# Kernel tuning notes

Measured on AMD Instinct MI355X. Metric: run time of the kernel, lower is better.

The kernel has to match this reference:

```python
import jax, jax.numpy as jnp
import numpy as np

H = 16       # num heads
HD = 64      # head dim
D = H * HD   # hidden size

def _rotate_half(x):
    x1, x2 = jnp.split(x, 2, axis=-1)
    return jnp.concatenate([-x2, x1], axis=-1)

def setup_inputs() -> dict:
    key = jax.random.key(0)
    ks = jax.random.split(key, 12)
    B, N, NP = 16, 1029, 1024  # batch, tokens (5 prefix + 1024 patches), patch tokens
    inp = {
        "hidden_states": jax.random.normal(ks[0], (B, N, D), dtype=jnp.float32),
        "sin": jax.random.uniform(ks[1], (NP, HD), dtype=jnp.float32, minval=-1.0, maxval=1.0),
        "cos": jax.random.uniform(ks[2], (NP, HD), dtype=jnp.float32, minval=-1.0, maxval=1.0),
        "Wq": jax.random.normal(ks[3], (D, D), dtype=jnp.float32) * 0.02,
        "bq": jnp.zeros((D,), dtype=jnp.float32),
        "Wk": jax.random.normal(ks[4], (D, D), dtype=jnp.float32) * 0.02,
        "bk": jnp.zeros((D,), dtype=jnp.float32),
        "Wv": jax.random.normal(ks[5], (D, D), dtype=jnp.float32) * 0.02,
        "bv": jnp.zeros((D,), dtype=jnp.float32),
        "Wo": jax.random.normal(ks[6], (D, D), dtype=jnp.float32) * 0.02,
        "bo": jnp.zeros((D,), dtype=jnp.float32),
    }
    return inp

def reference(hidden_states, sin, cos, Wq, bq, Wk, bk, Wv, bv, Wo, bo):
    B, N, _ = hidden_states.shape
    scaling = HD ** -0.5
    # qkv projections (nn.Linear: x @ W.T + b), split to heads: [B,H,N,HD]
    def proj(W, b):
        y = hidden_states @ W.T + b
        return y.reshape(B, N, H, HD).transpose(0, 2, 1, 3)
    q, k, v = proj(Wq, bq), proj(Wk, bk), proj(Wv, bv)
    # rotary pos emb on patch-token suffix only
    prefix = N - sin.shape[-2]
    def rope(x):
        xs = x[:, :, prefix:, :]
        xs = xs * cos + _rotate_half(xs) * sin
        return jnp.concatenate([x[:, :, :prefix, :], xs], axis=2)
    q, k = rope(q), rope(k)
    # eager attention: softmax in fp32
    attn = jnp.einsum("bhqd,bhkd->bhqk", q, k) * scaling
    attn = jax.nn.softmax(attn.astype(jnp.float32), axis=-1).astype(q.dtype)
    out = jnp.einsum("bhqk,bhkd->bhqd", attn, v)
    out = out.transpose(0, 2, 1, 3).reshape(B, N, D)
    return out @ Wo.T + bo
```

## Files before the change

### kernel.cpp

```cpp
#include <hip/hip_runtime.h>
#include <stdint.h>

#define H 16
#define HD 64
#define D 1024
#define NTOK 1029
#define BATCH 16
#define NPAD 1152
#define M_ROWS (BATCH*NTOK)
#define MPAD 16512
#define KB 1024
#define PREFIX 5

typedef unsigned short u16;
typedef __attribute__((ext_vector_type(8))) short short8;
typedef __attribute__((ext_vector_type(4))) short short4v;
typedef __attribute__((ext_vector_type(4))) float float4v;
typedef __attribute__((ext_vector_type(4))) unsigned int uint4v;

__device__ __forceinline__ u16 f2bf(float x) {
  unsigned int u = __float_as_uint(x);
  u += 0x7FFFu + ((u >> 16) & 1u);
  return (u16)(u >> 16);
}

__device__ __forceinline__ void gload16(const void* g, void* l) {
  __builtin_amdgcn_global_load_lds((const __attribute__((address_space(1))) void*)g,
                                   (__attribute__((address_space(3))) void*)l, 16, 0, 0);
}

__global__ __launch_bounds__(256) void cvt_A_kernel(const float* __restrict__ src,
                                                    u16* __restrict__ dst) {
  int idx = blockIdx.x * 256 + threadIdx.x;
  int m = idx >> 8, k = (idx & 255) * 4;
  float4v x = (float4v)0.f;
  if (m < M_ROWS) x = *(const float4v*)(src + (size_t)m * D + k);
  short4v o;
#pragma unroll
  for (int j = 0; j < 4; j++) o[j] = (short)f2bf(x[j]);
  *(short4v*)(dst + (size_t)m * D + k) = o;
}

__global__ __launch_bounds__(256) void cvt_W_kernel(
    const float* __restrict__ w0, const float* __restrict__ w1,
    const float* __restrict__ w2, const float* __restrict__ w3,
    u16* __restrict__ e0, u16* __restrict__ e1, u16* __restrict__ e2, u16* __restrict__ e3) {
  const float* src = (blockIdx.y == 0) ? w0 : (blockIdx.y == 1) ? w1 : (blockIdx.y == 2) ? w2 : w3;
  u16* dst = (blockIdx.y == 0) ? e0 : (blockIdx.y == 1) ? e1 : (blockIdx.y == 2) ? e2 : e3;
  int idx = blockIdx.x * 256 + threadIdx.x;
  int m = idx >> 8, k = (idx & 255) * 4;
  float4v x = *(const float4v*)(src + (size_t)m * D + k);
  short4v o;
#pragma unroll
  for (int j = 0; j < 4; j++) o[j] = (short)f2bf(x[j]);
  *(short4v*)(dst + (size_t)m * D + k) = o;
}

__device__ __forceinline__ void gemm_mainloop(const u16* __restrict__ A,
                                              const u16* __restrict__ Bw,
                                              u16* As, u16* Bs,
                                              int mtile, int ntile,
                                              float4v acc[4][4]) {
  const int tid = threadIdx.x;
  const int lane = tid & 63;
  const int wave = tid >> 6;
  const int wm = (wave >> 1) * 64;
  const int wn = (wave & 1) * 64;
  const int ar = lane & 15;
  const int kq = lane >> 4;
#pragma unroll
  for (int i = 0; i < 4; i++)
#pragma unroll
    for (int j = 0; j < 4; j++) acc[i][j] = (float4v)0.f;

  const size_t abase = (size_t)mtile * 128 * KB;
  const size_t bbase = (size_t)ntile * 128 * KB;
  for (int k0 = 0; k0 < KB; k0 += 64) {
    __syncthreads();
#pragma unroll
    for (int h = 0; h < 2; h++) {
#pragma unroll
      for (int i = 0; i < 2; i++) {
        int chunk = i * 256 + tid;
        gload16(A + abase + (size_t)(chunk >> 2) * KB + k0 + h * 32 + (chunk & 3) * 8,
                As + h * 4096 + (size_t)(i * 256 + (tid & ~63)) * 8);
        gload16(Bw + bbase + (size_t)(chunk >> 2) * KB + k0 + h * 32 + (chunk & 3) * 8,
                Bs + h * 4096 + (size_t)(i * 256 + (tid & ~63)) * 8);
      }
    }
    __syncthreads();
#pragma unroll
    for (int h = 0; h < 2; h++) {
      short8 af[4], bf[4];
#pragma unroll
      for (int ms = 0; ms < 4; ms++)
        af[ms] = *(const short8*)(As + h * 4096 + (wm + ms * 16 + ar) * 32 + kq * 8);
#pragma unroll
      for (int ns = 0; ns < 4; ns++)
        bf[ns] = *(const short8*)(Bs + h * 4096 + (wn + ns * 16 + ar) * 32 + kq * 8);
#pragma unroll
      for (int ms = 0; ms < 4; ms++)
#pragma unroll
        for (int ns = 0; ns < 4; ns++)
          acc[ms][ns] = __builtin_amdgcn_mfma_f32_16x16x32_bf16(af[ms], bf[ns], acc[ms][ns], 0, 0, 0);
    }
  }
}

__global__ __launch_bounds__(256) void gemm_qkv_kernel(
    const u16* __restrict__ A,
    const u16* __restrict__ Wqb, const u16* __restrict__ Wkb, const u16* __restrict__ Wvb,
    const float* __restrict__ bq, const float* __restrict__ bk, const float* __restrict__ bv,
    const float* __restrict__ sinp, const float* __restrict__ cosp,
    u16* __restrict__ qb, u16* __restrict__ kb, u16* __restrict__ vt) {
  __shared__ __align__(16) u16 As[2 * 128 * 32];
  __shared__ __align__(16) u16 Bs[2 * 128 * 32];
  int L = blockIdx.x;
  int t = (L & 7) * 387 + (L >> 3);
  int z = t / 1032;
  int r = t - z * 1032;
  const int mtile = r >> 3, ntile = r & 7;
  const u16* Bw = (z == 0) ? Wqb : (z == 1) ? Wkb : Wvb;
  const float* bias = (z == 0) ? bq : (z == 1) ? bk : bv;
  float4v acc[4][4];
  gemm_mainloop(A, Bw, As, Bs, mtile, ntile, acc);

  const int tid = threadIdx.x, lane = tid & 63, wave = tid >> 6;
  const int wm = (wave >> 1) * 64, wn = (wave & 1) * 64;
  const int ar = lane & 15, kq = lane >> 4;
#pragma unroll
  for (int ms = 0; ms < 4; ms++) {
#pragma unroll
    for (int r2 = 0; r2 < 4; r2++) {
      int grow = mtile * 128 + wm + ms * 16 + kq * 4 + r2;
      if (grow >= M_ROWS) continue;
      int b = grow / NTOK;
      int n = grow - b * NTOK;
      bool dorope = (z != 2) && (n >= PREFIX);
      int pos = n - PREFIX;
#pragma unroll
      for (int ns = 0; ns < 4; ns++) {
        int col = ntile * 128 + wn + ns * 16 + ar;
        int hh = col >> 6, d = col & 63;
        float y = acc[ms][ns][r2] + bias[col];
        if (z == 2) {
          vt[((size_t)(b * H + hh) * 64 + d) * NPAD + n] = f2bf(y);
          continue;
        }
        if (dorope) {
          float xp = acc[ms][ns ^ 2][r2] + bias[col ^ 32];
          float c = cosp[pos * HD + d], s = sinp[pos * HD + d];
          y = y * c + ((d < 32) ? -xp : xp) * s;
        }
        if (z == 0) y *= 0.125f;
        u16* outp = (z == 0) ? qb : kb;
        outp[((size_t)(b * H + hh) * NPAD + n) * 64 + d] = f2bf(y);
      }
    }
  }
}

#define SSHIFT 3.0f
#define NJT 17
__global__ __launch_bounds__(256) void attn_kernel(const u16* __restrict__ qb,
                                                   const u16* __restrict__ kb,
                                                   const u16* __restrict__ vt,
                                                   u16* __restrict__ ao) {
  __shared__ __align__(16) u16 sQ[128 * 72];
  __shared__ __align__(16) u16 sK[64 * 72];
  __shared__ __align__(16) u16 sV[64 * 72];
  const int tid = threadIdx.x, lane = tid & 63, wave = tid >> 6;
  const int ar = lane & 15, kq = lane >> 4;
  const int qt = blockIdx.x, hh = blockIdx.y, b = blockIdx.z;
  const int bh = b * H + hh;
  const u16* qbase = qb + (size_t)bh * NPAD * 64;
  const u16* kbase = kb + (size_t)bh * NPAD * 64;
  const u16* vbase = vt + (size_t)bh * 64 * NPAD;

#pragma unroll
  for (int i = 0; i < 4; i++) {
    int chunk = i * 256 + tid;
    int row = chunk >> 3, c = chunk & 7;
    *(uint4v*)(sQ + row * 72 + c * 8) =
        *(const uint4v*)(qbase + (size_t)(qt * 128 + row) * 64 + c * 8);
  }
  __syncthreads();
  short8 aq[2][2];
#pragma unroll
  for (int ms = 0; ms < 2; ms++)
#pragma unroll
    for (int ki = 0; ki < 2; ki++)
      aq[ms][ki] = *(const short8*)(sQ + (wave * 32 + ms * 16 + ar) * 72 + ki * 32 + kq * 8);
  u16* sP = sQ + wave * 32 * 72;

  float rs[2][4];
  float4v o_acc[2][4];
#pragma unroll
  for (int ms = 0; ms < 2; ms++)
#pragma unroll
    for (int r = 0; r < 4; r++) rs[ms][r] = 0.f;
#pragma unroll
  for (int ms = 0; ms < 2; ms++)
#pragma unroll
    for (int t = 0; t < 4; t++) o_acc[ms][t] = (float4v)0.f;

  for (int jt = 0; jt < NJT; jt++) {
    __syncthreads();
#pragma unroll
    for (int i = 0; i < 2; i++) {
      int chunk = i * 256 + tid;
      int row = chunk >> 3, c = chunk & 7;
      *(uint4v*)(sK + row * 72 + c * 8) =
          *(const uint4v*)(kbase + (size_t)(jt * 64 + row) * 64 + c * 8);
      *(uint4v*)(sV + row * 72 + c * 8) =
          *(const uint4v*)(vbase + (size_t)row * NPAD + jt * 64 + c * 8);
    }
    __syncthreads();

    float4v s[2][4];
#pragma unroll
    for (int ms = 0; ms < 2; ms++)
#pragma unroll
      for (int t = 0; t < 4; t++) s[ms][t] = (float4v)0.f;
#pragma unroll
    for (int ki = 0; ki < 2; ki++) {
#pragma unroll
      for (int t = 0; t < 4; t++) {
        short8 bk8 = *(const short8*)(sK + (t * 16 + ar) * 72 + ki * 32 + kq * 8);
#pragma unroll
        for (int ms = 0; ms < 2; ms++)
          s[ms][t] = __builtin_amdgcn_mfma_f32_16x16x32_bf16(aq[ms][ki], bk8, s[ms][t], 0, 0, 0);
      }
    }
    if (jt == NJT - 1) {
#pragma unroll
      for (int t = 0; t < 4; t++)
        if ((NJT - 1) * 64 + t * 16 + ar >= NTOK) {
#pragma unroll
          for (int ms = 0; ms < 2; ms++) s[ms][t] = (float4v)(-INFINITY);
        }
    }
    asm volatile("" ::: "memory");
#pragma unroll
    for (int ms = 0; ms < 2; ms++)
#pragma unroll
      for (int t = 0; t < 4; t++)
#pragma unroll
        for (int r = 0; r < 4; r++) {
          float p = __expf(s[ms][t][r] - SSHIFT);
          rs[ms][r] += p;
          sP[(ms * 16 + kq * 4 + r) * 72 + t * 16 + ar] = f2bf(p);
        }
    asm volatile("" ::: "memory");
#pragma unroll
    for (int ki = 0; ki < 2; ki++) {
#pragma unroll
      for (int ms = 0; ms < 2; ms++) {
        short8 ap = *(const short8*)(sP + (ms * 16 + ar) * 72 + ki * 32 + kq * 8);
#pragma unroll
        for (int t = 0; t < 4; t++) {
          short8 bv8 = *(const short8*)(sV + (t * 16 + ar) * 72 + ki * 32 + kq * 8);
          o_acc[ms][t] = __builtin_amdgcn_mfma_f32_16x16x32_bf16(ap, bv8, o_acc[ms][t], 0, 0, 0);
        }
      }
    }
  }
#pragma unroll
  for (int ms = 0; ms < 2; ms++)
#pragma unroll
    for (int r = 0; r < 4; r++) {
      float l = rs[ms][r];
#pragma unroll
      for (int off = 1; off < 16; off <<= 1) l += __shfl_xor(l, off, 64);
      int i = qt * 128 + wave * 32 + ms * 16 + kq * 4 + r;
      if (i >= NTOK) continue;
      float inv = 1.f / l;
      size_t mg = (size_t)b * NTOK + i;
#pragma unroll
      for (int t = 0; t < 4; t++)
        ao[mg * D + hh * 64 + t * 16 + ar] = f2bf(o_acc[ms][t][r] * inv);
    }
}

__global__ __launch_bounds__(256) void gemm_o_kernel(const u16* __restrict__ A,
                                                     const u16* __restrict__ Wob,
                                                     const float* __restrict__ bo,
                                                     float* __restrict__ out) {
  __shared__ __align__(16) u16 As[2 * 128 * 32];
  __shared__ __align__(16) u16 Bs[2 * 128 * 32];
  int L = blockIdx.x;
  int t = (L & 7) * 129 + (L >> 3);
  const int mtile = t >> 3, ntile = t & 7;
  float4v acc[4][4];
  gemm_mainloop(A, Wob, As, Bs, mtile, ntile, acc);
  const int tid = threadIdx.x, lane = tid & 63, wave = tid >> 6;
  const int wm = (wave >> 1) * 64, wn = (wave & 1) * 64;
  const int ar = lane & 15, kq = lane >> 4;
#pragma unroll
  for (int ms = 0; ms < 4; ms++)
#pragma unroll
    for (int r = 0; r < 4; r++) {
      int grow = mtile * 128 + wm + ms * 16 + kq * 4 + r;
      if (grow >= M_ROWS) continue;
#pragma unroll
      for (int ns = 0; ns < 4; ns++) {
        int col = ntile * 128 + wn + ns * 16 + ar;
        out[(size_t)grow * D + col] = acc[ms][ns][r] + bo[col];
      }
    }
}

extern "C" void kernel_launch(void* const* d_in, const int* in_sizes, int n_in,
                              void* d_out, int out_size, void* d_ws, size_t ws_size,
                              hipStream_t stream) {
  const float* hidden = (const float*)d_in[0];
  const float* sinp = (const float*)d_in[1];
  const float* cosp = (const float*)d_in[2];
  const float* Wq = (const float*)d_in[3]; const float* bq = (const float*)d_in[4];
  const float* Wk = (const float*)d_in[5]; const float* bk = (const float*)d_in[6];
  const float* Wv = (const float*)d_in[7]; const float* bv = (const float*)d_in[8];
  const float* Wo = (const float*)d_in[9]; const float* bo = (const float*)d_in[10];
  float* out = (float*)d_out;
  (void)in_sizes; (void)n_in; (void)out_size; (void)ws_size;

  char* ws = (char*)d_ws;
  size_t off = 0;
  auto carve = [&](size_t elems) {
    u16* p = (u16*)(ws + off);
    off += ((elems * 2 + 255) & ~(size_t)255);
    return p;
  };
  u16* A_bf = carve((size_t)MPAD * KB);
  u16* Wqb = carve((size_t)D * KB);
  u16* Wkb = carve((size_t)D * KB);
  u16* Wvb = carve((size_t)D * KB);
  u16* Wob = carve((size_t)D * KB);
  u16* q_b = carve((size_t)BATCH * H * NPAD * 64);
  u16* k_b = carve((size_t)BATCH * H * NPAD * 64);
  u16* v_t = carve((size_t)BATCH * H * NPAD * 64);

  hipLaunchKernelGGL(cvt_A_kernel, dim3(MPAD), dim3(256), 0, stream, hidden, A_bf);
  hipLaunchKernelGGL(cvt_W_kernel, dim3(1024, 4), dim3(256), 0, stream,
                     Wq, Wk, Wv, Wo, Wqb, Wkb, Wvb, Wob);
  hipLaunchKernelGGL(gemm_qkv_kernel, dim3(3096), dim3(256), 0, stream,
                     A_bf, Wqb, Wkb, Wvb, bq, bk, bv, sinp, cosp, q_b, k_b, v_t);
  hipLaunchKernelGGL(attn_kernel, dim3(9, H, BATCH), dim3(256), 0, stream, q_b, k_b, v_t, A_bf);
  hipLaunchKernelGGL(gemm_o_kernel, dim3(1032), dim3(256), 0, stream, A_bf, Wob, bo, out);
}
```

Measured before the change: 621.1 us.

## Store operands in MFMA fragment layout and load GEMM fragments directly from global

The conversion kernels and the attention output now write A and the weights in a pre-swizzled 16-row by 32-k fragment order, and the Q/K/V weights are packed into one buffer. The GEMM mainloop drops shared memory and barriers and loads each wave's MFMA fragments straight from global memory with register double buffering. The goal is to remove LDS staging and sync overhead. The cost is that operand reuse across waves in a block no longer happens on-chip, so L2 traffic per block increases. Block-to-tile mapping for the QKV GEMM is also changed to group N tiles per XCD.

```diff
diff --git a/kernel.cpp b/kernel.cpp
--- a/kernel.cpp
+++ b/kernel.cpp
@@ -24,10 +24,6 @@
   return (u16)(u >> 16);
 }
 
-__device__ __forceinline__ void gload16(const void* g, void* l) {
-  __builtin_amdgcn_global_load_lds((const __attribute__((address_space(1))) void*)g,
-                                   (__attribute__((address_space(3))) void*)l, 16, 0, 0);
-}
 
 __global__ __launch_bounds__(256) void cvt_A_kernel(const float* __restrict__ src,
                                                     u16* __restrict__ dst) {
@@ -38,96 +34,96 @@
   short4v o;
 #pragma unroll
   for (int j = 0; j < 4; j++) o[j] = (short)f2bf(x[j]);
-  *(short4v*)(dst + (size_t)m * D + k) = o;
+  int gm = m >> 4, rm = m & 15, gk = k >> 5, kq = (k >> 3) & 3, e = k & 7;
+  size_t off = (((size_t)gm * 32 + gk) * 64 + (rm + 16 * kq)) * 8 + e;
+  *(short4v*)(dst + off) = o;
 }
 
 __global__ __launch_bounds__(256) void cvt_W_kernel(
     const float* __restrict__ w0, const float* __restrict__ w1,
     const float* __restrict__ w2, const float* __restrict__ w3,
-    u16* __restrict__ e0, u16* __restrict__ e1, u16* __restrict__ e2, u16* __restrict__ e3) {
-  const float* src = (blockIdx.y == 0) ? w0 : (blockIdx.y == 1) ? w1 : (blockIdx.y == 2) ? w2 : w3;
-  u16* dst = (blockIdx.y == 0) ? e0 : (blockIdx.y == 1) ? e1 : (blockIdx.y == 2) ? e2 : e3;
+    u16* __restrict__ wqkv, u16* __restrict__ wo) {
+  const int y = blockIdx.y;
+  const float* src = (y == 0) ? w0 : (y == 1) ? w1 : (y == 2) ? w2 : w3;
   int idx = blockIdx.x * 256 + threadIdx.x;
   int m = idx >> 8, k = (idx & 255) * 4;
   float4v x = *(const float4v*)(src + (size_t)m * D + k);
   short4v o;
 #pragma unroll
   for (int j = 0; j < 4; j++) o[j] = (short)f2bf(x[j]);
-  *(short4v*)(dst + (size_t)m * D + k) = o;
-}
-
-__device__ __forceinline__ void gemm_mainloop(const u16* __restrict__ A,
-                                              const u16* __restrict__ Bw,
-                                              u16* As, u16* Bs,
-                                              int mtile, int ntile,
-                                              float4v acc[4][4]) {
-  const int tid = threadIdx.x;
-  const int lane = tid & 63;
-  const int wave = tid >> 6;
-  const int wm = (wave >> 1) * 64;
-  const int wn = (wave & 1) * 64;
-  const int ar = lane & 15;
-  const int kq = lane >> 4;
+  int gn = (y == 3) ? (m >> 4) : (y * 64 + (m >> 4));
+  int rn = m & 15, gk = k >> 5, kq = (k >> 3) & 3, e = k & 7;
+  u16* dst = (y == 3) ? wo : wqkv;
+  size_t off = (((size_t)gn * 32 + gk) * 64 + (rn + 16 * kq)) * 8 + e;
+  *(short4v*)(dst + off) = o;
+}
+
+__device__ __forceinline__ void gemm_frag_mainloop(const u16* __restrict__ A2,
+                                                   const u16* __restrict__ B2,
+                                                   int gm0, int gn0, int lane,
+                                                   float4v acc[4][4]) {
+  const u16* pa[4];
+  const u16* pb[4];
+#pragma unroll
+  for (int i = 0; i < 4; i++) {
+    pa[i] = A2 + (size_t)(gm0 + i) * (32 * 512) + lane * 8;
+    pb[i] = B2 + (size_t)(gn0 + i) * (32 * 512) + lane * 8;
+  }
 #pragma unroll
   for (int i = 0; i < 4; i++)
 #pragma unroll
     for (int j = 0; j < 4; j++) acc[i][j] = (float4v)0.f;
 
-  const size_t abase = (size_t)mtile * 128 * KB;
-  const size_t bbase = (size_t)ntile * 128 * KB;
-  for (int k0 = 0; k0 < KB; k0 += 64) {
-    __syncthreads();
-#pragma unroll
-    for (int h = 0; h < 2; h++) {
-#pragma unroll
-      for (int i = 0; i < 2; i++) {
-        int chunk = i * 256 + tid;
-        gload16(A + abase + (size_t)(chunk >> 2) * KB + k0 + h * 32 + (chunk & 3) * 8,
-                As + h * 4096 + (size_t)(i * 256 + (tid & ~63)) * 8);
-        gload16(Bw + bbase + (size_t)(chunk >> 2) * KB + k0 + h * 32 + (chunk & 3) * 8,
-                Bs + h * 4096 + (size_t)(i * 256 + (tid & ~63)) * 8);
-      }
-    }
-    __syncthreads();
-#pragma unroll
-    for (int h = 0; h < 2; h++) {
-      short8 af[4], bf[4];
-#pragma unroll
-      for (int ms = 0; ms < 4; ms++)
-        af[ms] = *(const short8*)(As + h * 4096 + (wm + ms * 16 + ar) * 32 + kq * 8);
+  short8 a0[4], b0[4], a1[4], b1[4];
+#pragma unroll
+  for (int i = 0; i < 4; i++) {
+    a0[i] = *(const short8*)(pa[i]);
+    b0[i] = *(const short8*)(pb[i]);
+  }
+#pragma unroll 2
+  for (int gk = 0; gk < 32; gk += 2) {
+#pragma unroll
+    for (int i = 0; i < 4; i++) {
+      a1[i] = *(const short8*)(pa[i] + (gk + 1) * 512);
+      b1[i] = *(const short8*)(pb[i] + (gk + 1) * 512);
+    }
+#pragma unroll
+    for (int ms = 0; ms < 4; ms++)
 #pragma unroll
       for (int ns = 0; ns < 4; ns++)
-        bf[ns] = *(const short8*)(Bs + h * 4096 + (wn + ns * 16 + ar) * 32 + kq * 8);
-#pragma unroll
-      for (int ms = 0; ms < 4; ms++)
-#pragma unroll
-        for (int ns = 0; ns < 4; ns++)
-          acc[ms][ns] = __builtin_amdgcn_mfma_f32_16x16x32_bf16(af[ms], bf[ns], acc[ms][ns], 0, 0, 0);
-    }
+        acc[ms][ns] = __builtin_amdgcn_mfma_f32_16x16x32_bf16(a0[ms], b0[ns], acc[ms][ns], 0, 0, 0);
+    if (gk + 2 < 32) {
+#pragma unroll
+      for (int i = 0; i < 4; i++) {
+        a0[i] = *(const short8*)(pa[i] + (gk + 2) * 512);
+        b0[i] = *(const short8*)(pb[i] + (gk + 2) * 512);
+      }
+    }
+#pragma unroll
+    for (int ms = 0; ms < 4; ms++)
+#pragma unroll
+      for (int ns = 0; ns < 4; ns++)
+        acc[ms][ns] = __builtin_amdgcn_mfma_f32_16x16x32_bf16(a1[ms], b1[ns], acc[ms][ns], 0, 0, 0);
   }
 }
 
 __global__ __launch_bounds__(256) void gemm_qkv_kernel(
-    const u16* __restrict__ A,
-    const u16* __restrict__ Wqb, const u16* __restrict__ Wkb, const u16* __restrict__ Wvb,
+    const u16* __restrict__ A2, const u16* __restrict__ Wqkv,
     const float* __restrict__ bq, const float* __restrict__ bk, const float* __restrict__ bv,
     const float* __restrict__ sinp, const float* __restrict__ cosp,
     u16* __restrict__ qb, u16* __restrict__ kb, u16* __restrict__ vt) {
-  __shared__ __align__(16) u16 As[2 * 128 * 32];
-  __shared__ __align__(16) u16 Bs[2 * 128 * 32];
-  int L = blockIdx.x;
-  int t = (L & 7) * 387 + (L >> 3);
-  int z = t / 1032;
-  int r = t - z * 1032;
-  const int mtile = r >> 3, ntile = r & 7;
-  const u16* Bw = (z == 0) ? Wqb : (z == 1) ? Wkb : Wvb;
+  const int L = blockIdx.x;
+  const int xcd = L & 7, i = L >> 3;
+  const int lt = i % 3, mtile = i / 3;
+  const int ntile = xcd * 3 + lt;
+  const int z = ntile >> 3;
   const float* bias = (z == 0) ? bq : (z == 1) ? bk : bv;
-  float4v acc[4][4];
-  gemm_mainloop(A, Bw, As, Bs, mtile, ntile, acc);
-
   const int tid = threadIdx.x, lane = tid & 63, wave = tid >> 6;
   const int wm = (wave >> 1) * 64, wn = (wave & 1) * 64;
   const int ar = lane & 15, kq = lane >> 4;
+  float4v acc[4][4];
+  gemm_frag_mainloop(A2, Wqkv, mtile * 8 + (wm >> 4), ntile * 8 + (wn >> 4), lane, acc);
+
 #pragma unroll
   for (int ms = 0; ms < 4; ms++) {
 #pragma unroll
@@ -140,7 +136,7 @@
       int pos = n - PREFIX;
 #pragma unroll
       for (int ns = 0; ns < 4; ns++) {
-        int col = ntile * 128 + wn + ns * 16 + ar;
+        int col = (ntile & 7) * 128 + wn + ns * 16 + ar;
         int hh = col >> 6, d = col & 63;
         float y = acc[ms][ns][r2] + bias[col];
         if (z == 2) {
@@ -275,27 +271,28 @@
       int i = qt * 128 + wave * 32 + ms * 16 + kq * 4 + r;
       if (i >= NTOK) continue;
       float inv = 1.f / l;
-      size_t mg = (size_t)b * NTOK + i;
-#pragma unroll
-      for (int t = 0; t < 4; t++)
-        ao[mg * D + hh * 64 + t * 16 + ar] = f2bf(o_acc[ms][t][r] * inv);
-    }
-}
-
-__global__ __launch_bounds__(256) void gemm_o_kernel(const u16* __restrict__ A,
-                                                     const u16* __restrict__ Wob,
+      int m = b * NTOK + i;
+      int gm = m >> 4, rm = m & 15;
+#pragma unroll
+      for (int t = 0; t < 4; t++) {
+        int col = hh * 64 + t * 16 + ar;
+        int gk = col >> 5, kqp = (col >> 3) & 3, e = col & 7;
+        ao[(((size_t)gm * 32 + gk) * 64 + (rm + 16 * kqp)) * 8 + e] = f2bf(o_acc[ms][t][r] * inv);
+      }
+    }
+}
+
+__global__ __launch_bounds__(256) void gemm_o_kernel(const u16* __restrict__ A2,
+                                                     const u16* __restrict__ Wo2,
                                                      const float* __restrict__ bo,
                                                      float* __restrict__ out) {
-  __shared__ __align__(16) u16 As[2 * 128 * 32];
-  __shared__ __align__(16) u16 Bs[2 * 128 * 32];
-  int L = blockIdx.x;
-  int t = (L & 7) * 129 + (L >> 3);
-  const int mtile = t >> 3, ntile = t & 7;
-  float4v acc[4][4];
-  gemm_mainloop(A, Wob, As, Bs, mtile, ntile, acc);
+  const int L = blockIdx.x;
+  const int ntile = L & 7, mtile = L >> 3;
   const int tid = threadIdx.x, lane = tid & 63, wave = tid >> 6;
   const int wm = (wave >> 1) * 64, wn = (wave & 1) * 64;
   const int ar = lane & 15, kq = lane >> 4;
+  float4v acc[4][4];
+  gemm_frag_mainloop(A2, Wo2, mtile * 8 + (wm >> 4), ntile * 8 + (wn >> 4), lane, acc);
 #pragma unroll
   for (int ms = 0; ms < 4; ms++)
 #pragma unroll
@@ -330,20 +327,18 @@
     off += ((elems * 2 + 255) & ~(size_t)255);
     return p;
   };
-  u16* A_bf = carve((size_t)MPAD * KB);
-  u16* Wqb = carve((size_t)D * KB);
-  u16* Wkb = carve((size_t)D * KB);
-  u16* Wvb = carve((size_t)D * KB);
-  u16* Wob = carve((size_t)D * KB);
+  u16* A_fg = carve((size_t)MPAD * KB);
+  u16* Wqkv = carve((size_t)3 * D * KB);
+  u16* Wo2 = carve((size_t)D * KB);
   u16* q_b = carve((size_t)BATCH * H * NPAD * 64);
   u16* k_b = carve((size_t)BATCH * H * NPAD * 64);
   u16* v_t = carve((size_t)BATCH * H * NPAD * 64);
 
-  hipLaunchKernelGGL(cvt_A_kernel, dim3(MPAD), dim3(256), 0, stream, hidden, A_bf);
+  hipLaunchKernelGGL(cvt_A_kernel, dim3(MPAD), dim3(256), 0, stream, hidden, A_fg);
   hipLaunchKernelGGL(cvt_W_kernel, dim3(1024, 4), dim3(256), 0, stream,
-                     Wq, Wk, Wv, Wo, Wqb, Wkb, Wvb, Wob);
+                     Wq, Wk, Wv, Wo, Wqkv, Wo2);
   hipLaunchKernelGGL(gemm_qkv_kernel, dim3(3096), dim3(256), 0, stream,
-                     A_bf, Wqb, Wkb, Wvb, bq, bk, bv, sinp, cosp, q_b, k_b, v_t);
-  hipLaunchKernelGGL(attn_kernel, dim3(9, H, BATCH), dim3(256), 0, stream, q_b, k_b, v_t, A_bf);
-  hipLaunchKernelGGL(gemm_o_kernel, dim3(1032), dim3(256), 0, stream, A_bf, Wob, bo, out);
-}
+                     A_fg, Wqkv, bq, bk, bv, sinp, cosp, q_b, k_b, v_t);
+  hipLaunchKernelGGL(attn_kernel, dim3(9, H, BATCH), dim3(256), 0, stream, q_b, k_b, v_t, A_fg);
+  hipLaunchKernelGGL(gemm_o_kernel, dim3(1032), dim3(256), 0, stream, A_fg, Wo2, bo, out);
+}
```

Result: slower. 690.3 us (+11.1%).
